# Optimization experiments

Hardware: AMD Instinct MI355X
Metric: run time of the kernel (lower is better)

## Reference

```python
import jax, jax.numpy as jnp
import numpy as np

N_GRAPHS = 8192
HIDDEN = 256
N_NODES = 500000


def setup_inputs() -> dict:
    key = jax.random.key(0)
    k1, k2, k3, k4, k5 = jax.random.split(key, 5)
    x = jax.random.normal(k1, (N_NODES, HIDDEN), dtype=jnp.float32)
    batch = jnp.sort(jax.random.randint(k2, (N_NODES,), 0, N_GRAPHS, dtype=jnp.int32))
    # attention MLP params: Linear(H,H) -> tanh -> Linear(H,1)
    s1 = 1.0 / np.sqrt(HIDDEN)
    W1 = jax.random.uniform(k3, (HIDDEN, HIDDEN), minval=-s1, maxval=s1, dtype=jnp.float32)
    b1 = jnp.zeros((HIDDEN,), dtype=jnp.float32)
    W2 = jax.random.uniform(k4, (HIDDEN, 1), minval=-s1, maxval=s1, dtype=jnp.float32)
    b2 = jnp.zeros((1,), dtype=jnp.float32)
    return {"x": x, "batch": batch, "W1": W1, "b1": b1, "W2": W2, "b2": b2}


def reference(x, batch, W1, b1, W2, b2):
    # attention logits: [N, 1]
    h = jnp.tanh(x @ W1 + b1)
    attn_logits = h @ W2 + b2  # [N, 1]
    e = jnp.exp(attn_logits)   # faithful: no max-subtraction in original
    # segment-sum of exp per graph, gathered back per node
    denom = jax.ops.segment_sum(e, batch, num_segments=N_GRAPHS)  # [G, 1]
    attn_weights = e / (denom[batch] + 1e-8)  # [N, 1]
    weighted_x = x * attn_weights             # [N, H]
    graph_embeddings = jax.ops.segment_sum(weighted_x, batch, num_segments=N_GRAPHS)  # [G, H]
    return graph_embeddings
```

## Files before the change

### kernel.cpp

```cpp
#include <hip/hip_runtime.h>

#define N_NODES  500000
#define HIDDEN   256
#define N_GRAPHS 8192
#define NTILES   (N_NODES / 32)
#define NWIN     (N_NODES / 16)
#define PROW     260

typedef float f32x4 __attribute__((ext_vector_type(4)));
typedef short s16x8 __attribute__((ext_vector_type(8)));

__device__ __forceinline__ unsigned short f2bf(float f) {
    unsigned int u = __float_as_uint(f);
    u += 0x7fffu + ((u >> 16) & 1u);
    return (unsigned short)(u >> 16);
}

__device__ __forceinline__ float bf2f(unsigned short s) {
    return __uint_as_float(((unsigned)s) << 16);
}

__global__ void prep_w1_kernel(const float* __restrict__ W1,
                               unsigned short* __restrict__ w1pack) {
    int tid  = blockIdx.x * 256 + threadIdx.x;
    int lane = tid & 63;
    int slot = tid >> 6;
    int wv   = slot >> 5;
    int kt   = (slot >> 2) & 7;
    int ntp  = slot & 3;
    int nt   = wv * 4 + ntp;
    int krow = kt * 32 + ((lane >> 4) & 3) * 8;
    int col  = nt * 16 + (lane & 15);
    unsigned short tmp[8];
#pragma unroll
    for (int j = 0; j < 8; ++j)
        tmp[j] = f2bf(W1[(size_t)(krow + j) * 256 + col]);
    *(uint4*)(w1pack + (size_t)tid * 8) = *(const uint4*)tmp;
}

__global__ void offsets_kernel(const int* __restrict__ batch,
                               int* __restrict__ offsEnd) {
    int g = blockIdx.x * 256 + threadIdx.x;
    if (g >= N_GRAPHS) return;
    int lo = 0, hi = N_NODES;
    while (lo < hi) {
        int mid = (lo + hi) >> 1;
        if (batch[mid] < g + 1) lo = mid + 1; else hi = mid;
    }
    offsEnd[g] = lo;
}

__launch_bounds__(256, 3)
__global__ void fused_kernel(const float* __restrict__ x,
                             const int*   __restrict__ batch,
                             const float* __restrict__ b1,
                             const float* __restrict__ W2,
                             const float* __restrict__ b2,
                             const unsigned short* __restrict__ w1pack,
                             float* __restrict__ preW,
                             float* __restrict__ sufW,
                             float* __restrict__ out) {
    __shared__ unsigned short xbf[32 * 256];
    __shared__ float plds[128];

    const int tid  = threadIdx.x;
    const int wave = tid >> 6;
    const int lane = tid & 63;
    const int cl   = lane & 15;
    const int kgrp = lane >> 4;
    const int base = blockIdx.x * 32;

#pragma unroll
    for (int i = 0; i < 4; ++i) {
        int v   = tid + i * 256;
        int row = v >> 5;
        int cu  = v & 31;
        const float* p = x + (size_t)(base + row) * HIDDEN + cu * 8;
        f32x4 a = *(const f32x4*)p;
        f32x4 c = *(const f32x4*)(p + 4);
        s16x8 w;
        w[0] = (short)f2bf(a[0]); w[1] = (short)f2bf(a[1]);
        w[2] = (short)f2bf(a[2]); w[3] = (short)f2bf(a[3]);
        w[4] = (short)f2bf(c[0]); w[5] = (short)f2bf(c[1]);
        w[6] = (short)f2bf(c[2]); w[7] = (short)f2bf(c[3]);
        *(s16x8*)(xbf + (size_t)(row * 32 + (cu ^ (row & 7))) * 8) = w;
    }

    const int wwin = wave & 1;
    const int wsW  = base + wwin * 16;
    int bval = batch[wsW + cl];
    const int bprev = (wsW > 0) ? batch[wsW - 1] : -1;
    const int bnext = (wsW + 16 < N_NODES) ? batch[wsW + 16] : -1;

    float b1c[4], w2c[4];
#pragma unroll
    for (int ntp = 0; ntp < 4; ++ntp) {
        int nt = wave * 4 + ntp;
        b1c[ntp] = b1[nt * 16 + cl];
        w2c[ntp] = W2[nt * 16 + cl];
    }
    const float b2v = b2[0];
    __syncthreads();

    float sj[2][4];
#pragma unroll
    for (int rt = 0; rt < 2; ++rt)
#pragma unroll
        for (int j = 0; j < 4; ++j) sj[rt][j] = 0.f;

#pragma unroll
    for (int pass = 0; pass < 4; ++pass) {
        f32x4 acc[2];
        acc[0] = (f32x4){0.f, 0.f, 0.f, 0.f};
        acc[1] = (f32x4){0.f, 0.f, 0.f, 0.f};

#pragma unroll
        for (int kt = 0; kt < 8; ++kt) {
            s16x8 bf = *(const s16x8*)(w1pack +
                ((size_t)(((wave * 8 + kt) * 4 + pass) * 64 + lane) << 3));
#pragma unroll
            for (int rt = 0; rt < 2; ++rt) {
                int row = rt * 16 + cl;
                int cu  = kt * 4 + kgrp;
                s16x8 af = *(const s16x8*)(xbf +
                    (size_t)(row * 32 + (cu ^ (row & 7))) * 8);
                acc[rt] = __builtin_amdgcn_mfma_f32_16x16x32_bf16(
                    af, bf, acc[rt], 0, 0, 0);
            }
        }
        float bb = b1c[pass];
        float ww = w2c[pass];
#pragma unroll
        for (int rt = 0; rt < 2; ++rt)
#pragma unroll
            for (int j = 0; j < 4; ++j) {
                float h = acc[rt][j] + bb;
                h = fminf(fmaxf(h, -15.f), 15.f);
                float e2 = __expf(2.f * h);
                float th = (e2 - 1.f) * __builtin_amdgcn_rcpf(e2 + 1.f);
                sj[rt][j] += th * ww;
            }
    }

#pragma unroll
    for (int m = 1; m < 16; m <<= 1)
#pragma unroll
        for (int rt = 0; rt < 2; ++rt)
#pragma unroll
            for (int j = 0; j < 4; ++j)
                sj[rt][j] += __shfl_xor(sj[rt][j], m, 64);
    if (cl == 0) {
#pragma unroll
        for (int rt = 0; rt < 2; ++rt)
#pragma unroll
            for (int j = 0; j < 4; ++j)
                plds[wave * 32 + rt * 16 + kgrp * 4 + j] = sj[rt][j];
    }
    __syncthreads();

    if (wave < 2) {
        const int wid = blockIdx.x * 2 + wave;
        int rr = wwin * 16 + cl;
        float logit = plds[rr] + plds[32 + rr] + plds[64 + rr] + plds[96 + rr] + b2v;
        float el = __expf(logit);

        const int gfirst = __shfl(bval, 0, 64);
        const int glast  = __shfl(bval, 15, 64);
        const bool eb = (bprev == gfirst);
        const bool ef = (bnext == glast);

        const int cuW  = lane >> 1;
        const int half = (lane & 1) * 4;

        f32x4 accv = {0.f, 0.f, 0.f, 0.f};
        float accden = 0.f;
        int gcur = gfirst, sl = 0;
#pragma unroll
        for (int r = 0; r < 16; ++r) {
            int   g  = __shfl(bval, r, 64);
            float er = __shfl(el, r, 64);
            if (g != gcur) {
                bool sb = (sl == 0) && eb;
                if (!sb) {
                    float d = accden + 1e-8f;
                    f32x4 res;
                    res[0] = accv[0] / d; res[1] = accv[1] / d;
                    res[2] = accv[2] / d; res[3] = accv[3] / d;
                    *(f32x4*)(out + (size_t)gcur * HIDDEN + lane * 4) = res;
                } else {
                    *(f32x4*)(preW + (size_t)wid * PROW + lane * 4) = accv;
                    if (lane == 0) preW[(size_t)wid * PROW + 256] = accden;
                }
                accv = (f32x4){0.f, 0.f, 0.f, 0.f};
                accden = 0.f;
                gcur = g; sl = r;
            }
            int rl = wwin * 16 + r;
            const unsigned short* u = xbf +
                (size_t)(rl * 32 + (cuW ^ (rl & 7))) * 8 + half;
            accv[0] += er * bf2f(u[0]);
            accv[1] += er * bf2f(u[1]);
            accv[2] += er * bf2f(u[2]);
            accv[3] += er * bf2f(u[3]);
            accden += er;
        }
        {
            bool sb = (sl == 0) && eb;
            if (!sb && !ef) {
                float d = accden + 1e-8f;
                f32x4 res;
                res[0] = accv[0] / d; res[1] = accv[1] / d;
                res[2] = accv[2] / d; res[3] = accv[3] / d;
                *(f32x4*)(out + (size_t)gcur * HIDDEN + lane * 4) = res;
            } else if (!sb && sl > 0) {
                *(f32x4*)(sufW + (size_t)wid * PROW + lane * 4) = accv;
                if (lane == 0) sufW[(size_t)wid * PROW + 256] = accden;
            } else {
                *(f32x4*)(preW + (size_t)wid * PROW + lane * 4) = accv;
                if (lane == 0) preW[(size_t)wid * PROW + 256] = accden;
            }
        }
    }
}

__launch_bounds__(256)
__global__ void combine_kernel(const float* __restrict__ preW,
                               const float* __restrict__ sufW,
                               const int* __restrict__ offsEnd,
                               float* __restrict__ out) {
    const int g    = blockIdx.x * 4 + (threadIdx.x >> 6);
    const int lane = threadIdx.x & 63;
    if (g >= N_GRAPHS) return;
    const int s = (g == 0) ? 0 : offsEnd[g - 1];
    const int e = offsEnd[g];
    if (e == s) {
        *(f32x4*)(out + (size_t)g * HIDDEN + lane * 4) = (f32x4){0.f, 0.f, 0.f, 0.f};
        return;
    }
    const int w0 = s >> 4, w1 = (e - 1) >> 4;
    if (w0 == w1) return;

    const float* row = (s > (w0 << 4)) ? sufW + (size_t)w0 * PROW
                                       : preW + (size_t)w0 * PROW;
    f32x4 acc = *(const f32x4*)(row + lane * 4);
    float den = row[256];
    for (int w = w0 + 1; w <= w1; ++w) {
        const float* pr = preW + (size_t)w * PROW;
        acc += *(const f32x4*)(pr + lane * 4);
        den += pr[256];
    }
    float d = den + 1e-8f;
    f32x4 res;
    res[0] = acc[0] / d; res[1] = acc[1] / d;
    res[2] = acc[2] / d; res[3] = acc[3] / d;
    *(f32x4*)(out + (size_t)g * HIDDEN + lane * 4) = res;
}

extern "C" void kernel_launch(void* const* d_in, const int* in_sizes, int n_in,
                              void* d_out, int out_size, void* d_ws, size_t ws_size,
                              hipStream_t stream) {
    const float* x     = (const float*)d_in[0];
    const int*   batch = (const int*)d_in[1];
    const float* W1    = (const float*)d_in[2];
    const float* b1    = (const float*)d_in[3];
    const float* W2    = (const float*)d_in[4];
    const float* b2    = (const float*)d_in[5];
    float* out = (float*)d_out;

    unsigned short* w1pack = (unsigned short*)d_ws;
    int*   offsEnd = (int*)((char*)d_ws + 131072);
    float* preW    = (float*)((char*)d_ws + 163840);
    float* sufW    = (float*)((char*)d_ws + 163840 + (size_t)NWIN * PROW * 4);

    prep_w1_kernel<<<32, 256, 0, stream>>>(W1, w1pack);
    offsets_kernel<<<32, 256, 0, stream>>>(batch, offsEnd);

    fused_kernel<<<NTILES, 256, 0, stream>>>(x, batch, b1, W2, b2, w1pack,
                                             preW, sufW, out);
    combine_kernel<<<(N_GRAPHS + 3) / 4, 256, 0, stream>>>(preW, sufW, offsEnd, out);
}
```

Baseline: 197.5 us.

## Split segment pooling across all four waves and simplify tanh epilogue

The pooling phase now runs on all four waves instead of two. Each wave handles one 16-row window and half of the hidden columns, with two floats per lane instead of four. Separately, the tanh-times-W2 epilogue is rewritten algebraically as sum(w2) - 2*w2/(e^{2h}+1), which drops the clamp and a multiply per element. The clamp removal relies on exp overflow to inf giving rcp of 0, which still behaves correctly. The pooling work is spread more evenly, at the cost of narrower stores and more shuffles.

```diff
diff --git a/kernel.cpp b/kernel.cpp
--- a/kernel.cpp
+++ b/kernel.cpp
@@ -8,6 +8,7 @@
 #define PROW     260
 
 typedef float f32x4 __attribute__((ext_vector_type(4)));
+typedef float f32x2 __attribute__((ext_vector_type(2)));
 typedef short s16x8 __attribute__((ext_vector_type(8)));
 
 __device__ __forceinline__ unsigned short f2bf(float f) {
@@ -86,8 +87,9 @@
         *(s16x8*)(xbf + (size_t)(row * 32 + (cu ^ (row & 7))) * 8) = w;
     }
 
-    const int wwin = wave & 1;
-    const int wsW  = base + wwin * 16;
+    const int wwin  = wave & 1;
+    const int chalf = wave >> 1;
+    const int wsW   = base + wwin * 16;
     int bval = batch[wsW + cl];
     const int bprev = (wsW > 0) ? batch[wsW - 1] : -1;
     const int bnext = (wsW + 16 < N_NODES) ? batch[wsW + 16] : -1;
@@ -102,11 +104,12 @@
     const float b2v = b2[0];
     __syncthreads();
 
+    const float wsum = w2c[0] + w2c[1] + w2c[2] + w2c[3];
     float sj[2][4];
 #pragma unroll
     for (int rt = 0; rt < 2; ++rt)
 #pragma unroll
-        for (int j = 0; j < 4; ++j) sj[rt][j] = 0.f;
+        for (int j = 0; j < 4; ++j) sj[rt][j] = wsum;
 
 #pragma unroll
     for (int pass = 0; pass < 4; ++pass) {
@@ -128,17 +131,16 @@
                     af, bf, acc[rt], 0, 0, 0);
             }
         }
-        float bb = b1c[pass];
-        float ww = w2c[pass];
+        float bb  = b1c[pass];
+        float ww2 = 2.f * w2c[pass];
 #pragma unroll
         for (int rt = 0; rt < 2; ++rt)
 #pragma unroll
             for (int j = 0; j < 4; ++j) {
-                float h = acc[rt][j] + bb;
-                h = fminf(fmaxf(h, -15.f), 15.f);
+                float h  = acc[rt][j] + bb;
                 float e2 = __expf(2.f * h);
-                float th = (e2 - 1.f) * __builtin_amdgcn_rcpf(e2 + 1.f);
-                sj[rt][j] += th * ww;
+                float rc = __builtin_amdgcn_rcpf(e2 + 1.f);
+                sj[rt][j] = fmaf(-ww2, rc, sj[rt][j]);
             }
     }
 
@@ -158,8 +160,8 @@
     }
     __syncthreads();
 
-    if (wave < 2) {
-        const int wid = blockIdx.x * 2 + wave;
+    {
+        const int wid = blockIdx.x * 2 + wwin;
         int rr = wwin * 16 + cl;
         float logit = plds[rr] + plds[32 + rr] + plds[64 + rr] + plds[96 + rr] + b2v;
         float el = __expf(logit);
@@ -169,10 +171,12 @@
         const bool eb = (bprev == gfirst);
         const bool ef = (bnext == glast);
 
-        const int cuW  = lane >> 1;
-        const int half = (lane & 1) * 4;
-
-        f32x4 accv = {0.f, 0.f, 0.f, 0.f};
+        const int c0  = chalf * 128 + lane * 2;
+        const int cuW = c0 >> 3;
+        const int off = c0 & 7;
+        const bool wden = (chalf == 0) && (lane == 0);
+
+        f32x2 accv = {0.f, 0.f};
         float accden = 0.f;
         int gcur = gfirst, sl = 0;
 #pragma unroll
@@ -183,41 +187,37 @@
                 bool sb = (sl == 0) && eb;
                 if (!sb) {
                     float d = accden + 1e-8f;
-                    f32x4 res;
+                    f32x2 res;
                     res[0] = accv[0] / d; res[1] = accv[1] / d;
-                    res[2] = accv[2] / d; res[3] = accv[3] / d;
-                    *(f32x4*)(out + (size_t)gcur * HIDDEN + lane * 4) = res;
+                    *(f32x2*)(out + (size_t)gcur * HIDDEN + c0) = res;
                 } else {
-                    *(f32x4*)(preW + (size_t)wid * PROW + lane * 4) = accv;
-                    if (lane == 0) preW[(size_t)wid * PROW + 256] = accden;
+                    *(f32x2*)(preW + (size_t)wid * PROW + c0) = accv;
+                    if (wden) preW[(size_t)wid * PROW + 256] = accden;
                 }
-                accv = (f32x4){0.f, 0.f, 0.f, 0.f};
+                accv = (f32x2){0.f, 0.f};
                 accden = 0.f;
                 gcur = g; sl = r;
             }
             int rl = wwin * 16 + r;
             const unsigned short* u = xbf +
-                (size_t)(rl * 32 + (cuW ^ (rl & 7))) * 8 + half;
+                (size_t)(rl * 32 + (cuW ^ (rl & 7))) * 8 + off;
             accv[0] += er * bf2f(u[0]);
             accv[1] += er * bf2f(u[1]);
-            accv[2] += er * bf2f(u[2]);
-            accv[3] += er * bf2f(u[3]);
             accden += er;
         }
         {
             bool sb = (sl == 0) && eb;
             if (!sb && !ef) {
                 float d = accden + 1e-8f;
-                f32x4 res;
+                f32x2 res;
                 res[0] = accv[0] / d; res[1] = accv[1] / d;
-                res[2] = accv[2] / d; res[3] = accv[3] / d;
-                *(f32x4*)(out + (size_t)gcur * HIDDEN + lane * 4) = res;
+                *(f32x2*)(out + (size_t)gcur * HIDDEN + c0) = res;
             } else if (!sb && sl > 0) {
-                *(f32x4*)(sufW + (size_t)wid * PROW + lane * 4) = accv;
-                if (lane == 0) sufW[(size_t)wid * PROW + 256] = accden;
+                *(f32x2*)(sufW + (size_t)wid * PROW + c0) = accv;
+                if (wden) sufW[(size_t)wid * PROW + 256] = accden;
             } else {
-                *(f32x4*)(preW + (size_t)wid * PROW + lane * 4) = accv;
-                if (lane == 0) preW[(size_t)wid * PROW + 256] = accden;
+                *(f32x2*)(preW + (size_t)wid * PROW + c0) = accv;
+                if (wden) preW[(size_t)wid * PROW + 256] = accden;
             }
         }
     }
```

Result: slower. 206.0 us (+4.3%).
